# Kernel optimization log

Measured on AMD Instinct MI355X. Metric: run time of the kernel, lower is better.

The kernel has to match this reference:

```python
import jax, jax.numpy as jnp
import numpy as np

HIDDEN = 768
HEADS = 12
DK = 64
DV = 64

def setup_inputs() -> dict:
    key = jax.random.key(0)
    k1, k2, k3, k4, k5, k6 = jax.random.split(key, 6)
    B, N = 4, 2048
    x = jax.random.normal(k1, (B, HIDDEN, N), dtype=jnp.float32)
    mask = jax.random.randint(k2, (B, N), 0, 2, dtype=jnp.int32)
    # xavier_uniform for Linear(hidden -> d): limit = sqrt(6/(hidden+d))
    def xavier(k, out_d, in_d, lead=()):
        lim = float(np.sqrt(6.0 / (in_d + out_d)))
        return jax.random.uniform(k, lead + (out_d, in_d), jnp.float32, -lim, lim)
    Wq = xavier(k3, DK, HIDDEN, (HEADS,))   # (H, d_k, hidden)
    Wk = xavier(k4, DK, HIDDEN, (HEADS,))
    Wv = xavier(k5, DV, HIDDEN, (HEADS,))
    Wo = xavier(k6, HIDDEN, HEADS * DV)     # (hidden, H*d_v)
    return {"x": x, "Wq": Wq, "Wk": Wk, "Wv": Wv, "Wo": Wo, "mask": mask}

def reference(x, Wq, Wk, Wv, Wo, mask):
    # x: (B, hidden, N) -> (B, N, hidden)
    xt = jnp.transpose(x, (0, 2, 1))
    q = jnp.einsum('bnc,hdc->bhnd', xt, Wq)  # (B,H,N,d_k)
    k = jnp.einsum('bnc,hdc->bhnd', xt, Wk)
    v = jnp.einsum('bnc,hdc->bhnd', xt, Wv)  # (B,H,N,d_v)
    scale = 1.0 / jnp.sqrt(jnp.asarray(DK, x.dtype))
    qk = jnp.einsum('bhnd,bhmd->bhnm', q, k) * scale  # (B,H,N,N)
    neg_inf = jnp.asarray(-jnp.inf, x.dtype)
    qk = jnp.where(mask[:, None, None, :] != 0, qk, neg_inf)  # mask key positions
    attn = jax.nn.softmax(qk, axis=-1)
    ctx = jnp.einsum('bhnm,bhmd->bhnd', attn, v)  # (B,H,N,d_v)
    B, H, N, D = ctx.shape
    combined = jnp.transpose(ctx, (0, 2, 1, 3)).reshape(B, N, H * D)  # cat over heads
    out = jnp.einsum('bnf,cf->bnc', combined, Wo)  # Linear(H*d_v -> hidden)
    return jnp.transpose(out, (0, 2, 1))  # (B, hidden, N)
```

## Files before the change

kernel.cpp:

```cpp
#include <hip/hip_runtime.h>

typedef _Float16 f16;
typedef __attribute__((ext_vector_type(8))) _Float16 f16x8;
typedef __attribute__((ext_vector_type(4))) _Float16 f16x4;
typedef __attribute__((ext_vector_type(4))) float f32x4;

#define DEVINL __device__ __forceinline__

DEVINL void gload16(const void* g, void* l) {
  __builtin_amdgcn_global_load_lds(
      (const __attribute__((address_space(1))) void*)g,
      (__attribute__((address_space(3))) void*)l, 16, 0, 0);
}

DEVINL f32x4 mfma16(f16x8 a, f16x8 b, f32x4 c) {
  return __builtin_amdgcn_mfma_f32_16x16x32_f16(a, b, c, 0, 0, 0);
}

__global__ __launch_bounds__(256) void convert_qkv(const float* __restrict__ wq,
                                                   const float* __restrict__ wk,
                                                   const float* __restrict__ wv,
                                                   f16* __restrict__ dst) {
  int seg = blockIdx.x / 576;
  int i = ((blockIdx.x % 576) * 256 + threadIdx.x) * 4;
  const float* src = seg == 0 ? wq : (seg == 1 ? wk : wv);
  f32x4 v = *(const f32x4*)(src + i);
  f16x4 o = {(f16)v[0], (f16)v[1], (f16)v[2], (f16)v[3]};
  *(f16x4*)(dst + seg * 589824 + i) = o;
}

__global__ __launch_bounds__(256) void convert_k(const float* __restrict__ src,
                                                 f16* __restrict__ dst, int n) {
  int i = (blockIdx.x * 256 + threadIdx.x) * 4;
  if (i + 3 < n) {
    f32x4 v = *(const f32x4*)(src + i);
    f16x4 o = {(f16)v[0], (f16)v[1], (f16)v[2], (f16)v[3]};
    *(f16x4*)(dst + i) = o;
  }
}

__global__ __launch_bounds__(256) void transpose_x(const float* __restrict__ x,
                                                   f16* __restrict__ xt) {
  __shared__ __attribute__((aligned(16))) f16 T[64 * 66];
  const int b = blockIdx.z, c0 = blockIdx.y * 64, n0 = blockIdx.x * 64;
  const int t = threadIdx.x;
  const float* xb = x + (size_t)b * 768 * 2048;
#pragma unroll
  for (int r = 0; r < 4; ++r) {
    int chunk = r * 256 + t;
    int row = chunk >> 4, c4 = (chunk & 15) * 4;
    f32x4 v = *(const f32x4*)&xb[(size_t)(c0 + row) * 2048 + n0 + c4];
#pragma unroll
    for (int e = 0; e < 4; ++e) T[row * 66 + c4 + e] = (f16)v[e];
  }
  __syncthreads();
  f16* xtb = xt + (size_t)b * 2048 * 768;
  int n = t >> 2, cp = (t & 3) * 16;
  __attribute__((aligned(16))) f16 vals[16];
#pragma unroll
  for (int j = 0; j < 16; ++j) vals[j] = T[(cp + j) * 66 + n];
  *(f16x8*)&xtb[(size_t)(n0 + n) * 768 + c0 + cp] = *(const f16x8*)&vals[0];
  *(f16x8*)&xtb[(size_t)(n0 + n) * 768 + c0 + cp + 8] = *(const f16x8*)&vals[8];
}

__global__ __launch_bounds__(256, 2)
void gemm_kernel(const f16* __restrict__ A, const f16* __restrict__ Bt,
                 f16* __restrict__ qkt, f16* __restrict__ vbuf,
                 float* __restrict__ outp, int kind) {
  constexpr int K = 768;
  const int b = blockIdx.z;
  const int n0 = blockIdx.x * 128;
  const int m0 = blockIdx.y * 128;
  const int t = threadIdx.x;
  const int lane = t & 63, w = t >> 6, g = lane >> 4, lo = lane & 15;
  const int wm = (w >> 1) * 64, wn = (w & 1) * 64;

  __shared__ __attribute__((aligned(16))) f16 smem[16384];
  f16* As = smem;
  f16* Bs = smem + 8192;

  const f16* Ab = A + (size_t)m0 * K;
  const f16* Bb = Bt + (size_t)b * 2048 * K + (size_t)n0 * K;

  const f32x4 zf = {0.f, 0.f, 0.f, 0.f};
  f32x4 acc[4][4];
#pragma unroll
  for (int i = 0; i < 4; ++i)
#pragma unroll
    for (int j = 0; j < 4; ++j) acc[i][j] = zf;

  for (int kt = 0; kt < K; kt += 64) {
    __syncthreads();
#pragma unroll
    for (int r = 0; r < 4; ++r) {
      int chunk = r * 256 + t;
      int row = chunk >> 3;
      int c8 = (chunk & 7) ^ (row & 7);
      gload16(Ab + (size_t)row * K + kt + c8 * 8, As + chunk * 8);
    }
#pragma unroll
    for (int r = 0; r < 4; ++r) {
      int chunk = r * 256 + t;
      int row = chunk >> 3;
      int c8 = (chunk & 7) ^ (row & 7);
      gload16(Bb + (size_t)row * K + kt + c8 * 8, Bs + chunk * 8);
    }
    __syncthreads();
#pragma unroll
    for (int kk = 0; kk < 2; ++kk) {
      f16x8 af[4], bfr[4];
#pragma unroll
      for (int i = 0; i < 4; ++i) {
        int row = wm + i * 16 + lo;
        af[i] = *(const f16x8*)&As[row * 64 + (((kk * 4 + g) ^ (row & 7)) * 8)];
      }
#pragma unroll
      for (int j = 0; j < 4; ++j) {
        int col = wn + j * 16 + lo;
        bfr[j] = *(const f16x8*)&Bs[col * 64 + (((kk * 4 + g) ^ (col & 7)) * 8)];
      }
#pragma unroll
      for (int i = 0; i < 4; ++i)
#pragma unroll
        for (int j = 0; j < 4; ++j)
          acc[i][j] = mfma16(af[i], bfr[j], acc[i][j]);
    }
  }

  if (kind == 1) {
    float* Cb = outp + (size_t)b * 768 * 2048;
#pragma unroll
    for (int i = 0; i < 4; ++i) {
      int row = m0 + wm + i * 16 + g * 4;
#pragma unroll
      for (int j = 0; j < 4; ++j) {
        int col = n0 + wn + j * 16 + lo;
#pragma unroll
        for (int r2 = 0; r2 < 4; ++r2)
          Cb[(size_t)(row + r2) * 2048 + col] = acc[i][j][r2];
      }
    }
  } else if (m0 >= 1536) {
    f16* Vb = vbuf + (size_t)b * 768 * 2048;
#pragma unroll
    for (int i = 0; i < 4; ++i) {
      int row = m0 - 1536 + wm + i * 16 + g * 4;
#pragma unroll
      for (int j = 0; j < 4; ++j) {
        int col = n0 + wn + j * 16 + lo;
#pragma unroll
        for (int r2 = 0; r2 < 4; ++r2)
          Vb[(size_t)(row + r2) * 2048 + col] = (f16)acc[i][j][r2];
      }
    }
  } else {
    __syncthreads();
    f16* T = smem;
#pragma unroll
    for (int i = 0; i < 4; ++i)
#pragma unroll
      for (int j = 0; j < 4; ++j) {
        int nl = wn + j * 16 + lo;
#pragma unroll
        for (int r2 = 0; r2 < 4; ++r2) {
          int ml = wm + i * 16 + g * 4 + r2;
          T[nl * 128 + (((ml >> 3) ^ (nl & 15)) * 8) + (ml & 7)] =
              (f16)acc[i][j][r2];
        }
      }
    __syncthreads();
    f16* Qb = qkt + (size_t)b * 2048 * 1536;
    int n = t >> 1, half = t & 1;
#pragma unroll
    for (int c = 0; c < 8; ++c) {
      int chunk = half * 8 + c;
      f16x8 v = *(const f16x8*)&T[n * 128 + ((chunk ^ (n & 15)) * 8)];
      *(f16x8*)&Qb[(size_t)(n0 + n) * 1536 + m0 + chunk * 8] = v;
    }
  }
}

__global__ __launch_bounds__(256, 3)
void attn_kernel(const f16* __restrict__ qkt, const f16* __restrict__ vbuf,
                 const int* __restrict__ mask, f16* __restrict__ ctxt) {
  const int bh = blockIdx.y;
  const int b = bh / 12, h = bh % 12;
  const int n0 = blockIdx.x * 128;
  const int t = threadIdx.x;
  const int lane = t & 63, w = t >> 6, g = lane >> 4, lo = lane & 15;

  __shared__ __attribute__((aligned(16))) f16 Kd[2][4096];
  __shared__ __attribute__((aligned(16))) f16 Vd[2][4096];
  __shared__ __attribute__((aligned(16))) f16 Ps[4][2048];
  __shared__ __attribute__((aligned(16))) f16 bias_s[2048];

  const f16* qb = qkt + (size_t)b * 2048 * 1536;
  const int* mb = mask + b * 2048;
#pragma unroll
  for (int r = 0; r < 8; ++r) {
    int i = r * 256 + t;
    bias_s[i] = (f16)(mb[i] ? 0.f : -60000.f);
  }

  constexpr float QS = 0.125f * 1.44269504088896f;
  f16x8 qa[2][2];
#pragma unroll
  for (int fm = 0; fm < 2; ++fm)
#pragma unroll
    for (int kk = 0; kk < 2; ++kk) {
      f16x8 v = *(const f16x8*)&qb[(size_t)(n0 + w * 32 + fm * 16 + lo) * 1536 +
                                   h * 64 + kk * 32 + g * 8];
#pragma unroll
      for (int e = 0; e < 8; ++e) v[e] = (f16)((float)v[e] * QS);
      qa[fm][kk] = v;
    }

  const f32x4 zf = {0.f, 0.f, 0.f, 0.f};
  f32x4 oacc[2][4];
  float mrun[2], lrun[2];
#pragma unroll
  for (int fm = 0; fm < 2; ++fm) {
#pragma unroll
    for (int fd = 0; fd < 4; ++fd) oacc[fm][fd] = zf;
    mrun[fm] = -3e38f;
    lrun[fm] = 0.f;
  }

  const f16* kb_g = qb + 768 + h * 64;
  const f16* vb_g = vbuf + (size_t)b * 768 * 2048 + (size_t)(h * 64) * 2048;
  f16* psw = &Ps[w][0];

#define STAGE_KV(BUF, M0)                                                     \
  {                                                                           \
    _Pragma("unroll") for (int r = 0; r < 2; ++r) {                           \
      int chunk = r * 256 + t;                                                \
      int row = chunk >> 3;                                                   \
      int c8 = (chunk & 7) ^ (row & 7);                                       \
      gload16(kb_g + (size_t)((M0) + row) * 1536 + c8 * 8,                    \
              &Kd[BUF][0] + chunk * 8);                                       \
    }                                                                         \
    _Pragma("unroll") for (int r = 0; r < 2; ++r) {                           \
      int chunk = r * 256 + t;                                                \
      int d = chunk >> 3;                                                     \
      int c8 = (chunk & 7) ^ (d & 7);                                         \
      gload16(vb_g + (size_t)d * 2048 + (M0) + c8 * 8, &Vd[BUF][0] + chunk * 8);\
    }                                                                         \
  }

  STAGE_KV(0, 0);
  __syncthreads();

  for (int mt = 0; mt < 32; ++mt) {
    const int cur = mt & 1;
    const int m0 = mt * 64;
    if (mt + 1 < 32) STAGE_KV(cur ^ 1, m0 + 64);

    const f16* Kb = &Kd[cur][0];
    const f16* Vb = &Vd[cur][0];

    f32x4 sacc[2][4];
#pragma unroll
    for (int fm = 0; fm < 2; ++fm)
#pragma unroll
      for (int fn = 0; fn < 4; ++fn) sacc[fm][fn] = zf;
#pragma unroll
    for (int kk = 0; kk < 2; ++kk)
#pragma unroll
      for (int fn = 0; fn < 4; ++fn) {
        int m = fn * 16 + lo;
        f16x8 kf = *(const f16x8*)&Kb[m * 64 + (((kk * 4 + g) ^ (m & 7)) * 8)];
        sacc[0][fn] = mfma16(kf, qa[0][kk], sacc[0][fn]);
        sacc[1][fn] = mfma16(kf, qa[1][kk], sacc[1][fn]);
      }

#pragma unroll
    for (int fn = 0; fn < 4; ++fn) {
      f16x4 b4 = *(const f16x4*)&bias_s[m0 + fn * 16 + g * 4];
      f32x4 ba = {(float)b4[0], (float)b4[1], (float)b4[2], (float)b4[3]};
      sacc[0][fn] += ba;
      sacc[1][fn] += ba;
    }

    f16x4 p16[2][4];
#pragma unroll
    for (int fm = 0; fm < 2; ++fm) {
      f32x4 vm = sacc[fm][0];
#pragma unroll
      for (int fn = 1; fn < 4; ++fn)
#pragma unroll
        for (int r = 0; r < 4; ++r) vm[r] = fmaxf(vm[r], sacc[fm][fn][r]);
      float mx = fmaxf(fmaxf(vm[0], vm[1]), fmaxf(vm[2], vm[3]));
      mx = fmaxf(mx, __shfl_xor(mx, 16, 64));
      mx = fmaxf(mx, __shfl_xor(mx, 32, 64));
      float mnew = fmaxf(mrun[fm], mx);
      float alpha = __builtin_amdgcn_exp2f(mrun[fm] - mnew);
      mrun[fm] = mnew;
      f32x4 vs_ = zf;
#pragma unroll
      for (int fn = 0; fn < 4; ++fn) {
        f32x4 pv;
#pragma unroll
        for (int r = 0; r < 4; ++r)
          pv[r] = __builtin_amdgcn_exp2f(sacc[fm][fn][r] - mnew);
        vs_ += pv;
        f16x4 ph = {(f16)pv[0], (f16)pv[1], (f16)pv[2], (f16)pv[3]};
        p16[fm][fn] = ph;
      }
      float rs = (vs_[0] + vs_[1]) + (vs_[2] + vs_[3]);
      rs += __shfl_xor(rs, 16, 64);
      rs += __shfl_xor(rs, 32, 64);
      lrun[fm] = lrun[fm] * alpha + rs;
#pragma unroll
      for (int fd = 0; fd < 4; ++fd) oacc[fm][fd] *= alpha;
    }

#pragma unroll
    for (int fm = 0; fm < 2; ++fm) {
      int q32 = fm * 16 + lo;
      int sw = q32 & 7;
#pragma unroll
      for (int fn = 0; fn < 4; ++fn) {
        int cq = fn * 2 + (g >> 1);
        *(f16x4*)&psw[q32 * 64 + ((cq ^ sw) * 8) + (g & 1) * 4] = p16[fm][fn];
      }
    }
#pragma unroll
    for (int kk = 0; kk < 2; ++kk) {
      f16x8 pa[2], vf[4];
#pragma unroll
      for (int fm = 0; fm < 2; ++fm) {
        int q32 = fm * 16 + lo;
        pa[fm] =
            *(const f16x8*)&psw[q32 * 64 + (((kk * 4 + g) ^ (q32 & 7)) * 8)];
      }
#pragma unroll
      for (int fd = 0; fd < 4; ++fd) {
        int d = fd * 16 + lo;
        vf[fd] = *(const f16x8*)&Vb[d * 64 + (((kk * 4 + g) ^ (d & 7)) * 8)];
      }
#pragma unroll
      for (int fm = 0; fm < 2; ++fm)
#pragma unroll
        for (int fd = 0; fd < 4; ++fd)
          oacc[fm][fd] = mfma16(vf[fd], pa[fm], oacc[fm][fd]);
    }

    __syncthreads();
  }

  f16* T2 = &Kd[0][0];
#pragma unroll
  for (int fm = 0; fm < 2; ++fm) {
    float rcp = 1.f / lrun[fm];
    int q = w * 32 + fm * 16 + lo;
    int sw = q & 7;
#pragma unroll
    for (int fd = 0; fd < 4; ++fd) {
      int c8 = fd * 2 + (g >> 1);
      f16x4 o4 = {(f16)(oacc[fm][fd][0] * rcp), (f16)(oacc[fm][fd][1] * rcp),
                  (f16)(oacc[fm][fd][2] * rcp), (f16)(oacc[fm][fd][3] * rcp)};
      *(f16x4*)&T2[q * 64 + ((c8 ^ sw) * 8) + (g & 1) * 4] = o4;
    }
  }
  __syncthreads();
  f16* cb = ctxt + (size_t)b * 2048 * 768;
  int qrow = t >> 1, half = t & 1;
#pragma unroll
  for (int c = 0; c < 4; ++c) {
    int c8 = half * 4 + c;
    f16x8 v = *(const f16x8*)&T2[qrow * 64 + ((c8 ^ (qrow & 7)) * 8)];
    *(f16x8*)&cb[(size_t)(n0 + qrow) * 768 + h * 64 + c8 * 8] = v;
  }
#undef STAGE_KV
}

extern "C" void kernel_launch(void* const* d_in, const int* in_sizes, int n_in,
                              void* d_out, int out_size, void* d_ws,
                              size_t ws_size, hipStream_t stream) {
  const float* x  = (const float*)d_in[0];
  const float* Wq = (const float*)d_in[1];
  const float* Wk = (const float*)d_in[2];
  const float* Wv = (const float*)d_in[3];
  const float* Wo = (const float*)d_in[4];
  const int* mask = (const int*)d_in[5];
  float* out = (float*)d_out;

  f16* Xt   = (f16*)d_ws;
  f16* Wcat = Xt + 6291456;
  f16* Wob  = Wcat + 1769472;
  f16* QKt  = Wob + 589824;
  f16* Vbuf = QKt + 12582912;
  f16* Ctxt = Xt;

  convert_qkv<<<1728, 256, 0, stream>>>(Wq, Wk, Wv, Wcat);
  convert_k<<<576, 256, 0, stream>>>(Wo, Wob, 589824);
  transpose_x<<<dim3(32, 12, 4), 256, 0, stream>>>(x, Xt);
  gemm_kernel<<<dim3(16, 18, 4), 256, 0, stream>>>(Wcat, Xt, QKt, Vbuf, nullptr, 0);
  attn_kernel<<<dim3(16, 48), 256, 0, stream>>>(QKt, Vbuf, mask, Ctxt);
  gemm_kernel<<<dim3(16, 6, 4), 256, 0, stream>>>(Wob, Ctxt, nullptr, nullptr, out, 1);
}
```

Baseline: 237.7 us.

## Merge weight conversions, lazy softmax rescale, bias-init accumulators, packed f16 convert

Merges the two weight-conversion kernels into one launch. In attention, the mask bias now seeds the score accumulators instead of being added after the MFMAs. The online softmax skips rescaling the running max and the output accumulators unless some lane's max grows by more than 8 (in log2 units), using a wave-wide __any. P values are converted to fp16 with packed cvt_pkrtz. Intent is to cut per-tile VALU and exp work and one launch; the lazy rescale lets unnormalized P reach up to 2^8, and round-toward-zero conversion slightly changes precision.

```diff
diff --git a/kernel.cpp b/kernel.cpp
--- a/kernel.cpp
+++ b/kernel.cpp
@@ -3,6 +3,7 @@
 typedef _Float16 f16;
 typedef __attribute__((ext_vector_type(8))) _Float16 f16x8;
 typedef __attribute__((ext_vector_type(4))) _Float16 f16x4;
+typedef __attribute__((ext_vector_type(2))) _Float16 f16x2;
 typedef __attribute__((ext_vector_type(4))) float f32x4;
 
 #define DEVINL __device__ __forceinline__
@@ -17,26 +18,23 @@
   return __builtin_amdgcn_mfma_f32_16x16x32_f16(a, b, c, 0, 0, 0);
 }
 
-__global__ __launch_bounds__(256) void convert_qkv(const float* __restrict__ wq,
-                                                   const float* __restrict__ wk,
-                                                   const float* __restrict__ wv,
-                                                   f16* __restrict__ dst) {
+DEVINL f16x2 cvt_pk(float a, float b) {
+  return __builtin_bit_cast(f16x2, __builtin_amdgcn_cvt_pkrtz(a, b));
+}
+
+__global__ __launch_bounds__(256) void convert_w(const float* __restrict__ wq,
+                                                 const float* __restrict__ wk,
+                                                 const float* __restrict__ wv,
+                                                 const float* __restrict__ wo,
+                                                 f16* __restrict__ wcat,
+                                                 f16* __restrict__ wob) {
   int seg = blockIdx.x / 576;
   int i = ((blockIdx.x % 576) * 256 + threadIdx.x) * 4;
-  const float* src = seg == 0 ? wq : (seg == 1 ? wk : wv);
+  const float* src = seg == 0 ? wq : (seg == 1 ? wk : (seg == 2 ? wv : wo));
+  f16* dst = seg < 3 ? wcat + seg * 589824 : wob;
   f32x4 v = *(const f32x4*)(src + i);
   f16x4 o = {(f16)v[0], (f16)v[1], (f16)v[2], (f16)v[3]};
-  *(f16x4*)(dst + seg * 589824 + i) = o;
-}
-
-__global__ __launch_bounds__(256) void convert_k(const float* __restrict__ src,
-                                                 f16* __restrict__ dst, int n) {
-  int i = (blockIdx.x * 256 + threadIdx.x) * 4;
-  if (i + 3 < n) {
-    f32x4 v = *(const f32x4*)(src + i);
-    f16x4 o = {(f16)v[0], (f16)v[1], (f16)v[2], (f16)v[3]};
-    *(f16x4*)(dst + i) = o;
-  }
+  *(f16x4*)(dst + i) = o;
 }
 
 __global__ __launch_bounds__(256) void transpose_x(const float* __restrict__ x,
@@ -260,9 +258,12 @@
 
     f32x4 sacc[2][4];
 #pragma unroll
-    for (int fm = 0; fm < 2; ++fm)
-#pragma unroll
-      for (int fn = 0; fn < 4; ++fn) sacc[fm][fn] = zf;
+    for (int fn = 0; fn < 4; ++fn) {
+      f16x4 b4 = *(const f16x4*)&bias_s[m0 + fn * 16 + g * 4];
+      f32x4 ba = {(float)b4[0], (float)b4[1], (float)b4[2], (float)b4[3]};
+      sacc[0][fn] = ba;
+      sacc[1][fn] = ba;
+    }
 #pragma unroll
     for (int kk = 0; kk < 2; ++kk)
 #pragma unroll
@@ -273,14 +274,6 @@
         sacc[1][fn] = mfma16(kf, qa[1][kk], sacc[1][fn]);
       }
 
-#pragma unroll
-    for (int fn = 0; fn < 4; ++fn) {
-      f16x4 b4 = *(const f16x4*)&bias_s[m0 + fn * 16 + g * 4];
-      f32x4 ba = {(float)b4[0], (float)b4[1], (float)b4[2], (float)b4[3]};
-      sacc[0][fn] += ba;
-      sacc[1][fn] += ba;
-    }
-
     f16x4 p16[2][4];
 #pragma unroll
     for (int fm = 0; fm < 2; ++fm) {
@@ -292,26 +285,32 @@
       float mx = fmaxf(fmaxf(vm[0], vm[1]), fmaxf(vm[2], vm[3]));
       mx = fmaxf(mx, __shfl_xor(mx, 16, 64));
       mx = fmaxf(mx, __shfl_xor(mx, 32, 64));
-      float mnew = fmaxf(mrun[fm], mx);
-      float alpha = __builtin_amdgcn_exp2f(mrun[fm] - mnew);
-      mrun[fm] = mnew;
+      if (__any(mx > mrun[fm] + 8.f)) {
+        float mnew = fmaxf(mrun[fm], mx);
+        float alpha = __builtin_amdgcn_exp2f(mrun[fm] - mnew);
+        mrun[fm] = mnew;
+        lrun[fm] *= alpha;
+#pragma unroll
+        for (int fd = 0; fd < 4; ++fd) oacc[fm][fd] *= alpha;
+      }
+      float mcur = mrun[fm];
       f32x4 vs_ = zf;
 #pragma unroll
       for (int fn = 0; fn < 4; ++fn) {
         f32x4 pv;
 #pragma unroll
         for (int r = 0; r < 4; ++r)
-          pv[r] = __builtin_amdgcn_exp2f(sacc[fm][fn][r] - mnew);
+          pv[r] = __builtin_amdgcn_exp2f(sacc[fm][fn][r] - mcur);
         vs_ += pv;
-        f16x4 ph = {(f16)pv[0], (f16)pv[1], (f16)pv[2], (f16)pv[3]};
+        f16x2 plo = cvt_pk(pv[0], pv[1]);
+        f16x2 phi = cvt_pk(pv[2], pv[3]);
+        f16x4 ph = {plo[0], plo[1], phi[0], phi[1]};
         p16[fm][fn] = ph;
       }
       float rs = (vs_[0] + vs_[1]) + (vs_[2] + vs_[3]);
       rs += __shfl_xor(rs, 16, 64);
       rs += __shfl_xor(rs, 32, 64);
-      lrun[fm] = lrun[fm] * alpha + rs;
-#pragma unroll
-      for (int fd = 0; fd < 4; ++fd) oacc[fm][fd] *= alpha;
+      lrun[fm] += rs;
     }
 
 #pragma unroll
@@ -392,8 +391,7 @@
   f16* Vbuf = QKt + 12582912;
   f16* Ctxt = Xt;
 
-  convert_qkv<<<1728, 256, 0, stream>>>(Wq, Wk, Wv, Wcat);
-  convert_k<<<576, 256, 0, stream>>>(Wo, Wob, 589824);
+  convert_w<<<2304, 256, 0, stream>>>(Wq, Wk, Wv, Wo, Wcat, Wob);
   transpose_x<<<dim3(32, 12, 4), 256, 0, stream>>>(x, Xt);
   gemm_kernel<<<dim3(16, 18, 4), 256, 0, stream>>>(Wcat, Xt, QKt, Vbuf, nullptr, 0);
   attn_kernel<<<dim3(16, 48), 256, 0, stream>>>(QKt, Vbuf, mask, Ctxt);
```

New measurement: 231.1 us. 1.03x faster.
